# Kernel optimization log

Measured on AMD Instinct MI355X. Metric: run time of the kernel, lower is better.

## Reference

```python
import jax, jax.numpy as jnp
import numpy as np

N_NODES = 100000
N_EDGES = 6400000
IN_NODE = 6
IN_EDGE = 1
HID = 10
OUT = 2


def setup_inputs() -> dict:
    key = jax.random.key(0)
    ks = jax.random.split(key, 8)
    x = jax.random.normal(ks[0], (N_NODES, IN_NODE), dtype=jnp.float32)
    edge_index = jax.random.randint(ks[1], (2, N_EDGES), 0, N_NODES, dtype=jnp.int64)
    edge_attr = jax.random.normal(ks[2], (N_EDGES, IN_EDGE), dtype=jnp.float32)
    edge_attr_T = jax.random.normal(ks[3], (N_EDGES, IN_EDGE), dtype=jnp.float32)
    in_dim = 2 * IN_NODE + IN_EDGE  # 13
    W1 = jax.random.normal(ks[4], (in_dim, HID), dtype=jnp.float32) / np.sqrt(in_dim)
    b1 = jnp.zeros((HID,), dtype=jnp.float32)
    W2 = jax.random.normal(ks[5], (HID, OUT), dtype=jnp.float32) / np.sqrt(HID)
    b2 = jnp.zeros((OUT,), dtype=jnp.float32)
    return {"x": x, "edge_index": edge_index, "edge_attr": edge_attr,
            "edge_attr_T": edge_attr_T, "W1": W1, "b1": b1, "W2": W2, "b2": b2}


def _mlp(feat, W1, b1, W2, b2):
    h = jax.nn.relu(feat @ W1 + b1)
    return h @ W2 + b2


def reference(x, edge_index, edge_attr, edge_attr_T, W1, b1, W2, b2):
    src = edge_index[0]
    tgt = edge_index[1]
    x_src = x[src]  # [E, 6]
    x_tgt = x[tgt]  # [E, 6]
    feat_fwd = jnp.concatenate([x_src, x_tgt, edge_attr], axis=-1)      # [E, 13]
    feat_rev = jnp.concatenate([x_tgt, x_src, edge_attr_T], axis=-1)    # [E, 13]
    out = _mlp(feat_fwd, W1, b1, W2, b2) + _mlp(feat_rev, W1, b1, W2, b2)
    out = out * 0.5
    out = jax.nn.softmax(out, axis=1)
    return out[:, -1:]  # [E, 1]
```

## Files before the change

### kernel.cpp

```cpp
#include <hip/hip_runtime.h>
#include <hip/hip_fp16.h>


typedef _Float16 half2_t __attribute__((ext_vector_type(2)));
typedef _Float16 half8_t __attribute__((ext_vector_type(8)));
typedef float    float2_v __attribute__((ext_vector_type(2)));
typedef int      int2_v   __attribute__((ext_vector_type(2)));

union h2u { __half2 h; unsigned u; half2_t v; };

__global__ void prep(const float* __restrict__ W1, const float* __restrict__ b1,
                     const float* __restrict__ W2, const float* __restrict__ b2,
                     const float* __restrict__ x, float* __restrict__ wsf, int N) {
    int t = blockIdx.x * 256 + threadIdx.x;
    if (t < N) {
        const float2* xr = (const float2*)x;
        float2 a0 = xr[3 * t], a1 = xr[3 * t + 1], a2 = xr[3 * t + 2];
        union { __half2 h[4]; float4 f; } pk;
        pk.h[0] = __floats2half2_rn(a0.x, a0.y);
        pk.h[1] = __floats2half2_rn(a1.x, a1.y);
        pk.h[2] = __floats2half2_rn(a2.x, a2.y);
        pk.h[3] = __floats2half2_rn(0.0f, 0.0f);
        ((float4*)((char*)wsf + 4096))[t] = pk.f;
    }
    if (blockIdx.x == 0) {
        unsigned* wsu = (unsigned*)wsf;
        int u = threadIdx.x;
        if (u < 10) wsf[u] = b1[u];
        if (u == 0) wsf[10] = b2[1] - b2[0];
        if (u < 30) {
            int k = u / 10, j = u % 10;
            float a0 = W1[(2 * k) * 10 + j],     c0 = W1[(2 * k + 6) * 10 + j];
            float a1 = W1[(2 * k + 1) * 10 + j], c1 = W1[(2 * k + 7) * 10 + j];
            h2u p, m;
            p.h = __floats2half2_rn(0.5f * (a0 + c0), 0.5f * (a1 + c1));
            m.h = __floats2half2_rn(0.5f * (a0 - c0), 0.5f * (a1 - c1));
            wsu[16 + u] = p.u;
            wsu[48 + u] = m.u;
        }
        if (u < 5) {
            h2u a, b;
            a.h = __floats2half2_rn(W1[120 + 2 * u], W1[120 + 2 * u + 1]);
            b.h = __floats2half2_rn(0.5f * (W2[(2 * u) * 2 + 1] - W2[(2 * u) * 2]),
                                    0.5f * (W2[(2 * u + 1) * 2 + 1] - W2[(2 * u + 1) * 2]));
            wsu[80 + u] = a.u;
            wsu[88 + u] = b.u;
        }
    }
}

static __device__ __forceinline__ float fdot2(half2_t a, half2_t b, float c) {
#if __has_builtin(__builtin_amdgcn_fdot2)
    return __builtin_amdgcn_fdot2(a, b, c, false);
#else
    return fmaf((float)a[0], (float)b[0], fmaf((float)a[1], (float)b[1], c));
#endif
}

static __device__ __forceinline__ half2_t h2bc(const unsigned* wsu, int idx) {
    h2u t; t.u = wsu[idx]; return t.v;
}

static __device__ __forceinline__ float edge_one(half8_t rs, half8_t rt,
                                                 float fea, float feaT,
                                                 const float* __restrict__ wsf,
                                                 const unsigned* __restrict__ wsu) {
    half8_t sv8 = rs + rt;
    half8_t dv8 = rs - rt;
    half2_t sv[3] = { __builtin_shufflevector(sv8, sv8, 0, 1),
                      __builtin_shufflevector(sv8, sv8, 2, 3),
                      __builtin_shufflevector(sv8, sv8, 4, 5) };
    half2_t dv[3] = { __builtin_shufflevector(dv8, dv8, 0, 1),
                      __builtin_shufflevector(dv8, dv8, 2, 3),
                      __builtin_shufflevector(dv8, dv8, 4, 5) };

    float cacc[10], macc[10];
#pragma unroll
    for (int j = 0; j < 10; ++j) { cacc[j] = wsf[j]; macc[j] = 0.0f; }
#pragma unroll
    for (int k = 0; k < 3; ++k) {
#pragma unroll
        for (int j = 0; j < 10; ++j) {
            cacc[j] = fdot2(sv[k], h2bc(wsu, 16 + k * 10 + j), cacc[j]);
            macc[j] = fdot2(dv[k], h2bc(wsu, 48 + k * 10 + j), macc[j]);
        }
    }

    _Float16 feah  = (_Float16)fea,  feaTh = (_Float16)feaT;
    half2_t fea2  = { feah,  feah  };
    half2_t feaT2 = { feaTh, feaTh };
    half2_t zero2 = { (_Float16)0.0f, (_Float16)0.0f };

    float z = wsf[10];
#pragma unroll
    for (int jp = 0; jp < 5; ++jp) {
        half2_t c2 = { (_Float16)cacc[2 * jp], (_Float16)cacc[2 * jp + 1] };
        half2_t m2 = { (_Float16)macc[2 * jp], (_Float16)macc[2 * jp + 1] };
        half2_t w12 = h2bc(wsu, 80 + jp);
        half2_t af2 = __builtin_elementwise_fma(fea2,  w12, c2 + m2);
        half2_t ar2 = __builtin_elementwise_fma(feaT2, w12, c2 - m2);
        half2_t h2  = __builtin_elementwise_max(af2, zero2) +
                      __builtin_elementwise_max(ar2, zero2);
        z = fdot2(h2, h2bc(wsu, 88 + jp), z);
    }
    return 1.0f / (1.0f + __expf(-z));
}

__launch_bounds__(256, 8)
__global__ void edge_mlp(const half8_t* __restrict__ xp, const int* __restrict__ ei,
                         const float* __restrict__ ea, const float* __restrict__ eaT,
                         const float* __restrict__ wsf, float* __restrict__ out, int E) {
    const unsigned* wsu = (const unsigned*)wsf;
    int g = blockIdx.x * 256 + threadIdx.x;
    int e0 = 2 * g;
    if (e0 + 1 < E) {
        int2_v   s2 = __builtin_nontemporal_load((const int2_v*)(ei + e0));
        int2_v   t2 = __builtin_nontemporal_load((const int2_v*)(ei + E + e0));
        float2_v fa = __builtin_nontemporal_load((const float2_v*)(ea + e0));
        float2_v fT = __builtin_nontemporal_load((const float2_v*)(eaT + e0));
        half8_t rs0 = xp[s2[0]], rt0 = xp[t2[0]];
        half8_t rs1 = xp[s2[1]], rt1 = xp[t2[1]];
        float2_v r;
        r[0] = edge_one(rs0, rt0, fa[0], fT[0], wsf, wsu);
        r[1] = edge_one(rs1, rt1, fa[1], fT[1], wsf, wsu);
        __builtin_nontemporal_store(r, (float2_v*)(out + e0));
    } else if (e0 < E) {
        int si = ei[e0], ti = ei[E + e0];
        float r = edge_one(xp[si], xp[ti], ea[e0], eaT[e0], wsf, wsu);
        out[e0] = r;
    }
}

extern "C" void kernel_launch(void* const* d_in, const int* in_sizes, int n_in,
                              void* d_out, int out_size, void* d_ws, size_t ws_size,
                              hipStream_t stream) {
    const float* x   = (const float*)d_in[0];
    const int*   ei  = (const int*)d_in[1];
    const float* ea  = (const float*)d_in[2];
    const float* eaT = (const float*)d_in[3];
    const float* W1  = (const float*)d_in[4];
    const float* b1  = (const float*)d_in[5];
    const float* W2  = (const float*)d_in[6];
    const float* b2  = (const float*)d_in[7];
    float* out = (float*)d_out;
    float* ws  = (float*)d_ws;
    int E = in_sizes[2];
    int N = in_sizes[0] / 6;

    int pblocks = (N + 255) / 256;
    prep<<<pblocks, 256, 0, stream>>>(W1, b1, W2, b2, x, ws, N);

    const half8_t* xp = (const half8_t*)((char*)d_ws + 4096);
    int nthreads = (E + 1) / 2;
    int blocks = (nthreads + 255) / 256;
    edge_mlp<<<blocks, 256, 0, stream>>>(xp, ei, ea, eaT, ws, out, E);
}
```

Baseline: 197.8 us.

## Process four edges per thread with batched sc0 gathers via inline asm

Each thread now handles four edges, using 128-bit vector loads for the indices and edge attributes and a single 128-bit store for the results. The eight node-feature gathers are issued as inline-asm global_load_dwordx4 with the sc0 cache hint, followed by one explicit s_waitcnt, so that more gathers are in flight at once. Launch bounds drop to 4 blocks per CU to allow more registers. The trade-off is lower occupancy and more register pressure, and the hand-placed waitcnt prevents the compiler from scheduling those loads itself.

After: 190.5 us (median of 2 runs). 1.04x faster.

```diff
diff --git a/kernel.cpp b/kernel.cpp
--- a/kernel.cpp
+++ b/kernel.cpp
@@ -2,10 +2,10 @@
 #include <hip/hip_fp16.h>
 
 
-typedef _Float16 half2_t __attribute__((ext_vector_type(2)));
-typedef _Float16 half8_t __attribute__((ext_vector_type(8)));
-typedef float    float2_v __attribute__((ext_vector_type(2)));
-typedef int      int2_v   __attribute__((ext_vector_type(2)));
+typedef _Float16 half2_t  __attribute__((ext_vector_type(2)));
+typedef _Float16 half8_t  __attribute__((ext_vector_type(8)));
+typedef float    float4_v __attribute__((ext_vector_type(4)));
+typedef int      int4_v   __attribute__((ext_vector_type(4)));
 
 union h2u { __half2 h; unsigned u; half2_t v; };
 
@@ -61,6 +61,13 @@
     h2u t; t.u = wsu[idx]; return t.v;
 }
 
+static __device__ __forceinline__ half8_t gather16_sc0(const half8_t* base, int idx) {
+    half8_t r;
+    const half8_t* p = base + idx;
+    asm volatile("global_load_dwordx4 %0, %1, off sc0" : "=v"(r) : "v"(p));
+    return r;
+}
+
 static __device__ __forceinline__ float edge_one(half8_t rs, half8_t rt,
                                                  float fea, float feaT,
                                                  const float* __restrict__ wsf,
@@ -106,28 +113,45 @@
     return 1.0f / (1.0f + __expf(-z));
 }
 
-__launch_bounds__(256, 8)
+__launch_bounds__(256, 4)
 __global__ void edge_mlp(const half8_t* __restrict__ xp, const int* __restrict__ ei,
                          const float* __restrict__ ea, const float* __restrict__ eaT,
                          const float* __restrict__ wsf, float* __restrict__ out, int E) {
     const unsigned* wsu = (const unsigned*)wsf;
     int g = blockIdx.x * 256 + threadIdx.x;
-    int e0 = 2 * g;
-    if (e0 + 1 < E) {
-        int2_v   s2 = __builtin_nontemporal_load((const int2_v*)(ei + e0));
-        int2_v   t2 = __builtin_nontemporal_load((const int2_v*)(ei + E + e0));
-        float2_v fa = __builtin_nontemporal_load((const float2_v*)(ea + e0));
-        float2_v fT = __builtin_nontemporal_load((const float2_v*)(eaT + e0));
-        half8_t rs0 = xp[s2[0]], rt0 = xp[t2[0]];
-        half8_t rs1 = xp[s2[1]], rt1 = xp[t2[1]];
-        float2_v r;
-        r[0] = edge_one(rs0, rt0, fa[0], fT[0], wsf, wsu);
-        r[1] = edge_one(rs1, rt1, fa[1], fT[1], wsf, wsu);
-        __builtin_nontemporal_store(r, (float2_v*)(out + e0));
-    } else if (e0 < E) {
-        int si = ei[e0], ti = ei[E + e0];
-        float r = edge_one(xp[si], xp[ti], ea[e0], eaT[e0], wsf, wsu);
-        out[e0] = r;
+    int e0 = 4 * g;
+    if (e0 + 3 < E) {
+        int4_v   s4 = __builtin_nontemporal_load((const int4_v*)(ei + e0));
+        int4_v   t4 = __builtin_nontemporal_load((const int4_v*)(ei + E + e0));
+        float4_v a4 = __builtin_nontemporal_load((const float4_v*)(ea + e0));
+        float4_v T4 = __builtin_nontemporal_load((const float4_v*)(eaT + e0));
+
+        half8_t rs0 = gather16_sc0(xp, s4[0]);
+        half8_t rt0 = gather16_sc0(xp, t4[0]);
+        half8_t rs1 = gather16_sc0(xp, s4[1]);
+        half8_t rt1 = gather16_sc0(xp, t4[1]);
+        half8_t rs2 = gather16_sc0(xp, s4[2]);
+        half8_t rt2 = gather16_sc0(xp, t4[2]);
+        half8_t rs3 = gather16_sc0(xp, s4[3]);
+        half8_t rt3 = gather16_sc0(xp, t4[3]);
+        asm volatile("s_waitcnt vmcnt(0)"
+                     : "+v"(rs0), "+v"(rt0), "+v"(rs1), "+v"(rt1),
+                       "+v"(rs2), "+v"(rt2), "+v"(rs3), "+v"(rt3)
+                     :: "memory");
+
+        float4_v r;
+        r[0] = edge_one(rs0, rt0, a4[0], T4[0], wsf, wsu);
+        r[1] = edge_one(rs1, rt1, a4[1], T4[1], wsf, wsu);
+        r[2] = edge_one(rs2, rt2, a4[2], T4[2], wsf, wsu);
+        r[3] = edge_one(rs3, rt3, a4[3], T4[3], wsf, wsu);
+        __builtin_nontemporal_store(r, (float4_v*)(out + e0));
+    } else {
+        for (int e = e0; e < E; ++e) {
+            int si = ei[e], ti = ei[E + e];
+            half8_t rs = ((const half8_t*)xp)[si];
+            half8_t rt = ((const half8_t*)xp)[ti];
+            out[e] = edge_one(rs, rt, ea[e], eaT[e], wsf, wsu);
+        }
     }
 }
 
@@ -151,7 +175,7 @@
     prep<<<pblocks, 256, 0, stream>>>(W1, b1, W2, b2, x, ws, N);
 
     const half8_t* xp = (const half8_t*)((char*)d_ws + 4096);
-    int nthreads = (E + 1) / 2;
+    int nthreads = (E + 3) / 4;
     int blocks = (nthreads + 255) / 256;
     edge_mlp<<<blocks, 256, 0, stream>>>(xp, ei, ea, eaT, ws, out, E);
 }
```

## Convert edge kernel to persistent grid-stride loop with software-pipelined gathers

Applied to the files above, without the earlier changes.

Replaces the one-thread-per-edge-pair launch with a fixed grid of 1024 blocks that loops over pairs in a grid-stride pattern. Each iteration prefetches the edge indices two steps ahead and the node-feature gathers one step ahead, so memory latency overlaps with the MLP arithmetic. Launch bounds drop to 4 blocks per SM to leave room for the extra live registers. The risks are lower occupancy and possibly too few blocks to fill the device, plus clamped redundant loads at the tail.

After: 202.5 us. 1.02x slower.

```diff
diff --git a/kernel.cpp b/kernel.cpp
--- a/kernel.cpp
+++ b/kernel.cpp
@@ -2,8 +2,8 @@
 #include <hip/hip_fp16.h>
 
 
-typedef _Float16 half2_t __attribute__((ext_vector_type(2)));
-typedef _Float16 half8_t __attribute__((ext_vector_type(8)));
+typedef _Float16 half2_t  __attribute__((ext_vector_type(2)));
+typedef _Float16 half8_t  __attribute__((ext_vector_type(8)));
 typedef float    float2_v __attribute__((ext_vector_type(2)));
 typedef int      int2_v   __attribute__((ext_vector_type(2)));
 
@@ -106,28 +106,62 @@
     return 1.0f / (1.0f + __expf(-z));
 }
 
-__launch_bounds__(256, 8)
+__launch_bounds__(256, 4)
 __global__ void edge_mlp(const half8_t* __restrict__ xp, const int* __restrict__ ei,
                          const float* __restrict__ ea, const float* __restrict__ eaT,
                          const float* __restrict__ wsf, float* __restrict__ out, int E) {
     const unsigned* wsu = (const unsigned*)wsf;
-    int g = blockIdx.x * 256 + threadIdx.x;
-    int e0 = 2 * g;
-    if (e0 + 1 < E) {
-        int2_v   s2 = __builtin_nontemporal_load((const int2_v*)(ei + e0));
-        int2_v   t2 = __builtin_nontemporal_load((const int2_v*)(ei + E + e0));
-        float2_v fa = __builtin_nontemporal_load((const float2_v*)(ea + e0));
-        float2_v fT = __builtin_nontemporal_load((const float2_v*)(eaT + e0));
-        half8_t rs0 = xp[s2[0]], rt0 = xp[t2[0]];
-        half8_t rs1 = xp[s2[1]], rt1 = xp[t2[1]];
+    const int T = gridDim.x * blockDim.x;
+    const int g = blockIdx.x * blockDim.x + threadIdx.x;
+    const int npairs = E >> 1;
+
+    if ((E & 1) && g == 0) {
+        int e = E - 1;
+        out[e] = edge_one(xp[ei[e]], xp[ei[E + e]], ea[e], eaT[e], wsf, wsu);
+    }
+    if (npairs == 0) return;
+
+    const int nit = (npairs + T - 1) / T;
+    const int plim = npairs - 1;
+
+    int pA = min(g, plim);
+    int2_v   sA = __builtin_nontemporal_load((const int2_v*)(ei + 2 * pA));
+    int2_v   tA = __builtin_nontemporal_load((const int2_v*)(ei + E + 2 * pA));
+    float2_v aA = __builtin_nontemporal_load((const float2_v*)(ea + 2 * pA));
+    float2_v TA = __builtin_nontemporal_load((const float2_v*)(eaT + 2 * pA));
+    int pB = min(g + T, plim);
+    int2_v   sB = __builtin_nontemporal_load((const int2_v*)(ei + 2 * pB));
+    int2_v   tB = __builtin_nontemporal_load((const int2_v*)(ei + E + 2 * pB));
+    float2_v aB = __builtin_nontemporal_load((const float2_v*)(ea + 2 * pB));
+    float2_v TB = __builtin_nontemporal_load((const float2_v*)(eaT + 2 * pB));
+
+    half8_t r0A = xp[sA[0]];
+    half8_t r1A = xp[tA[0]];
+    half8_t r2A = xp[sA[1]];
+    half8_t r3A = xp[tA[1]];
+
+    for (int it = 0; it < nit; ++it) {
+        half8_t r0B = xp[sB[0]];
+        half8_t r1B = xp[tB[0]];
+        half8_t r2B = xp[sB[1]];
+        half8_t r3B = xp[tB[1]];
+
+        int pC = min(g + (it + 2) * T, plim);
+        int2_v   sC = __builtin_nontemporal_load((const int2_v*)(ei + 2 * pC));
+        int2_v   tC = __builtin_nontemporal_load((const int2_v*)(ei + E + 2 * pC));
+        float2_v aC = __builtin_nontemporal_load((const float2_v*)(ea + 2 * pC));
+        float2_v TC = __builtin_nontemporal_load((const float2_v*)(eaT + 2 * pC));
+
         float2_v r;
-        r[0] = edge_one(rs0, rt0, fa[0], fT[0], wsf, wsu);
-        r[1] = edge_one(rs1, rt1, fa[1], fT[1], wsf, wsu);
-        __builtin_nontemporal_store(r, (float2_v*)(out + e0));
-    } else if (e0 < E) {
-        int si = ei[e0], ti = ei[E + e0];
-        float r = edge_one(xp[si], xp[ti], ea[e0], eaT[e0], wsf, wsu);
-        out[e0] = r;
+        r[0] = edge_one(r0A, r1A, aA[0], TA[0], wsf, wsu);
+        r[1] = edge_one(r2A, r3A, aA[1], TA[1], wsf, wsu);
+        int p = g + it * T;
+        if (p < npairs)
+            __builtin_nontemporal_store(r, (float2_v*)(out + 2 * p));
+
+        sA = sB; tA = tB; aA = aB; TA = TB;
+        r0A = r0B; r1A = r1B; r2A = r2B; r3A = r3B;
+        sB = sC; tB = tC; aB = aC; TB = TC;
     }
 }
 
@@ -151,7 +185,5 @@
     prep<<<pblocks, 256, 0, stream>>>(W1, b1, W2, b2, x, ws, N);
 
     const half8_t* xp = (const half8_t*)((char*)d_ws + 4096);
-    int nthreads = (E + 1) / 2;
-    int blocks = (nthreads + 255) / 256;
-    edge_mlp<<<blocks, 256, 0, stream>>>(xp, ei, ea, eaT, ws, out, E);
+    edge_mlp<<<1024, 256, 0, stream>>>(xp, ei, ea, eaT, ws, out, E);
 }
```

## Gather node features via global_load_lds into LDS with persistent grid-stride waves

Applied to the files above, without the earlier changes.

Replaces direct register gathers of fp16 node rows with the global_load_lds builtin, which writes 16 bytes per lane straight into a per-wave LDS slot that is then read back. The kernel becomes persistent: 2048 blocks of four waves stride over 64-edge groups, one edge per lane instead of two. This aims to cut VGPR pressure and launch overhead, but adds a full vmcnt(0) wait per group that serialises gathers with compute and gives up the two-edges-per-thread memory-level parallelism.

Result: slower. 210.2 us (+6.3%).

```diff
diff --git a/kernel.cpp b/kernel.cpp
--- a/kernel.cpp
+++ b/kernel.cpp
@@ -2,10 +2,8 @@
 #include <hip/hip_fp16.h>
 
 
-typedef _Float16 half2_t __attribute__((ext_vector_type(2)));
-typedef _Float16 half8_t __attribute__((ext_vector_type(8)));
-typedef float    float2_v __attribute__((ext_vector_type(2)));
-typedef int      int2_v   __attribute__((ext_vector_type(2)));
+typedef _Float16 half2_t  __attribute__((ext_vector_type(2)));
+typedef _Float16 half8_t  __attribute__((ext_vector_type(8)));
 
 union h2u { __half2 h; unsigned u; half2_t v; };
 
@@ -61,6 +59,21 @@
     h2u t; t.u = wsu[idx]; return t.v;
 }
 
+typedef __attribute__((address_space(3))) void lds_void_t;
+typedef __attribute__((address_space(1))) void gbl_void_t;
+
+static __device__ __forceinline__ void gather16_to_lds(const void* gaddr,
+                                                       void* lds_base, int lane) {
+#if __has_builtin(__builtin_amdgcn_global_load_lds)
+    (void)lane;
+    __builtin_amdgcn_global_load_lds((const gbl_void_t*)(unsigned long long)gaddr,
+                                     (lds_void_t*)(unsigned)(unsigned long long)lds_base,
+                                     16, 0, 0);
+#else
+    *(half8_t*)((char*)lds_base + lane * 16) = *(const half8_t*)gaddr;
+#endif
+}
+
 static __device__ __forceinline__ float edge_one(half8_t rs, half8_t rt,
                                                  float fea, float feaT,
                                                  const float* __restrict__ wsf,
@@ -110,24 +123,30 @@
 __global__ void edge_mlp(const half8_t* __restrict__ xp, const int* __restrict__ ei,
                          const float* __restrict__ ea, const float* __restrict__ eaT,
                          const float* __restrict__ wsf, float* __restrict__ out, int E) {
+    __shared__ uint4 lds_all[512];
     const unsigned* wsu = (const unsigned*)wsf;
-    int g = blockIdx.x * 256 + threadIdx.x;
-    int e0 = 2 * g;
-    if (e0 + 1 < E) {
-        int2_v   s2 = __builtin_nontemporal_load((const int2_v*)(ei + e0));
-        int2_v   t2 = __builtin_nontemporal_load((const int2_v*)(ei + E + e0));
-        float2_v fa = __builtin_nontemporal_load((const float2_v*)(ea + e0));
-        float2_v fT = __builtin_nontemporal_load((const float2_v*)(eaT + e0));
-        half8_t rs0 = xp[s2[0]], rt0 = xp[t2[0]];
-        half8_t rs1 = xp[s2[1]], rt1 = xp[t2[1]];
-        float2_v r;
-        r[0] = edge_one(rs0, rt0, fa[0], fT[0], wsf, wsu);
-        r[1] = edge_one(rs1, rt1, fa[1], fT[1], wsf, wsu);
-        __builtin_nontemporal_store(r, (float2_v*)(out + e0));
-    } else if (e0 < E) {
-        int si = ei[e0], ti = ei[E + e0];
-        float r = edge_one(xp[si], xp[ti], ea[e0], eaT[e0], wsf, wsu);
-        out[e0] = r;
+    const int wid  = threadIdx.x >> 6;
+    const int lane = threadIdx.x & 63;
+    char* wbase = (char*)lds_all + wid * 2048;
+
+    const int ngroups = (E + 63) >> 6;
+    const int gstride = gridDim.x * 4;
+    for (int g = blockIdx.x * 4 + wid; g < ngroups; g += gstride) {
+        int e  = (g << 6) + lane;
+        int ec = min(e, E - 1);
+        int   si  = __builtin_nontemporal_load(ei + ec);
+        int   ti  = __builtin_nontemporal_load(ei + E + ec);
+        float fea = __builtin_nontemporal_load(ea + ec);
+        float feT = __builtin_nontemporal_load(eaT + ec);
+
+        gather16_to_lds(xp + si, wbase, lane);
+        gather16_to_lds(xp + ti, wbase + 1024, lane);
+        asm volatile("s_waitcnt vmcnt(0)" ::: "memory");
+
+        half8_t rs = *(const half8_t*)(wbase + lane * 16);
+        half8_t rt = *(const half8_t*)(wbase + 1024 + lane * 16);
+        float r = edge_one(rs, rt, fea, feT, wsf, wsu);
+        if (e < E) __builtin_nontemporal_store(r, out + e);
     }
 }
 
@@ -151,7 +170,5 @@
     prep<<<pblocks, 256, 0, stream>>>(W1, b1, W2, b2, x, ws, N);
 
     const half8_t* xp = (const half8_t*)((char*)d_ws + 4096);
-    int nthreads = (E + 1) / 2;
-    int blocks = (nthreads + 255) / 256;
-    edge_mlp<<<blocks, 256, 0, stream>>>(xp, ei, ea, eaT, ws, out, E);
+    edge_mlp<<<2048, 256, 0, stream>>>(xp, ei, ea, eaT, ws, out, E);
 }
```
